# Kernel tuning notes

Measured on AMD Instinct MI355X. Metric: run time of the kernel, lower is better.

## Reference

```python
import jax, jax.numpy as jnp
import numpy as np
import math

N_NODES = 100000
N_EDGES = 3200000
IN_DIM = 256
HID_DIM = 256
OUT_DIM = 64
K1 = 2
P_DECAY = 1.0


def setup_inputs() -> dict:
    key = jax.random.key(0)
    k1, k2, k3, k4, k5, k6, k7 = jax.random.split(key, 7)
    x = jax.random.normal(k1, (N_NODES, IN_DIM), dtype=jnp.float32)
    edge_src = jax.random.randint(k2, (N_EDGES,), 0, N_NODES, dtype=jnp.int32)
    edge_dst = jax.random.randint(k3, (N_EDGES,), 0, N_NODES, dtype=jnp.int32)
    # Linear params (fc of conv1 and conv2), torch default init scale
    s1 = 1.0 / math.sqrt(IN_DIM)
    s2 = 1.0 / math.sqrt(HID_DIM)
    W1 = jax.random.uniform(k4, (IN_DIM, HID_DIM), jnp.float32, -s1, s1)
    b1 = jax.random.uniform(k5, (HID_DIM,), jnp.float32, -s1, s1)
    W2 = jax.random.uniform(k6, (HID_DIM, OUT_DIM), jnp.float32, -s2, s2)
    b2 = jax.random.uniform(k7, (OUT_DIM,), jnp.float32, -s2, s2)
    return {"x": x, "edge_src": edge_src, "edge_dst": edge_dst,
            "W1": W1, "b1": b1, "W2": W2, "b2": b2}


def _kprop_aggregate(x, src, dst, K, p, add_self_loops):
    """gcn_norm + K-hop propagation with exp(-p) decay per extra hop."""
    n = x.shape[0]
    if add_self_loops:
        loop = jnp.arange(n, dtype=src.dtype)
        src = jnp.concatenate([src, loop])
        dst = jnp.concatenate([dst, loop])
    # symmetric gcn normalization: w_ij = d_i^-1/2 * d_j^-1/2
    deg = jax.ops.segment_sum(jnp.ones_like(dst, dtype=x.dtype), dst, num_segments=n)
    dinv = jnp.where(deg > 0, jax.lax.rsqrt(jnp.maximum(deg, 1e-12)), 0.0)
    w = dinv[dst] * dinv[src]  # [E]
    coeff = 1.0
    for _ in range(K):
        msg = w[:, None] * x[src]                      # gather + scale  [E, D]
        x = jax.ops.segment_sum(msg, dst, num_segments=n) * coeff  # scatter-add [N, D]
        coeff = coeff * math.exp(-p)
    return x


def reference(x, edge_src, edge_dst, W1, b1, W2, b2):
    src = edge_src.astype(jnp.int32)
    dst = edge_dst.astype(jnp.int32)
    # conv1: KProp(K=2, gcn) -> no self loops in gcn_norm (add_self_loops = K==1)
    h = _kprop_aggregate(x, src, dst, K=K1, p=P_DECAY, add_self_loops=False)
    h = h @ W1 + b1
    h = jax.nn.selu(h)
    # dropout p=0.0 (eval-equivalent): identity
    # conv2: KProp(K=1, gcn) -> self loops added in gcn_norm
    h = _kprop_aggregate(h, src, dst, K=1, p=P_DECAY, add_self_loops=True)
    h = h @ W2 + b2
    return jax.nn.log_softmax(h, axis=1)
```

## Files before the change

kernel.cpp:

```cpp
#include <hip/hip_runtime.h>
#include <math.h>

static constexpr int IN_DIM_C  = 256;
static constexpr int HID_DIM_C = 256;
static constexpr int OUT_DIM_C = 64;
static constexpr float EXP_NEG1   = 0.36787944117144233f;
static constexpr float SELU_ALPHA = 1.6732632423543772f;
static constexpr float SELU_SCALE = 1.0507009873554805f;

static constexpr int NBLK  = 256;
static constexpr int NBUCK = 256;
static constexpr int BSH   = 9;
static constexpr int BMASK = (1 << BSH) - 1;

typedef __attribute__((ext_vector_type(4))) float f32x4;
typedef __attribute__((ext_vector_type(8))) short bf16x8;

__device__ __forceinline__ unsigned short bf1(float f) {
    unsigned int u = __float_as_uint(f);
    u = u + 0x7FFFu + ((u >> 16) & 1u);
    return (unsigned short)(u >> 16);
}
__device__ __forceinline__ unsigned int bfpack2(float lo, float hi) {
    return (unsigned int)bf1(lo) | ((unsigned int)bf1(hi) << 16);
}
__device__ __forceinline__ float fb(unsigned short h) {
    return __uint_as_float(((unsigned int)h) << 16);
}

__global__ __launch_bounds__(256) void k_hist(const int* __restrict__ dst,
                                              int* __restrict__ counts, int E) {
    __shared__ int hist[NBUCK];
    int tid = threadIdx.x, blk = blockIdx.x;
    hist[tid] = 0;
    __syncthreads();
    int ch = (E + NBLK - 1) / NBLK;
    int beg = blk * ch, end = min(beg + ch, E);
    for (int i = beg + tid; i < end; i += 256)
        atomicAdd(&hist[dst[i] >> BSH], 1);
    __syncthreads();
    counts[tid * NBLK + blk] = hist[tid];
}

__global__ void k_scan1(const int* __restrict__ in, int* __restrict__ out,
                        int* __restrict__ part, int n) {
    __shared__ int sm[256];
    int tid = threadIdx.x, idx = blockIdx.x * 256 + tid;
    int v = (idx < n) ? in[idx] : 0;
    sm[tid] = v; __syncthreads();
    #pragma unroll
    for (int o = 1; o < 256; o <<= 1) {
        int t = (tid >= o) ? sm[tid - o] : 0;
        __syncthreads();
        sm[tid] += t;
        __syncthreads();
    }
    if (idx < n) out[idx] = sm[tid] - v;
    if (tid == 255) part[blockIdx.x] = sm[255];
}

__global__ void k_scan2(int* __restrict__ part, int NB) {
    __shared__ int sm[512];
    int tid = threadIdx.x;
    int v = (tid < NB) ? part[tid] : 0;
    sm[tid] = v; __syncthreads();
    for (int o = 1; o < 512; o <<= 1) {
        int t = (tid >= o) ? sm[tid - o] : 0;
        __syncthreads();
        sm[tid] += t;
        __syncthreads();
    }
    if (tid < NB) part[tid] = sm[tid] - v;
}

__global__ void k_scan3b(int* __restrict__ v, const int* __restrict__ part, int n) {
    int idx = blockIdx.x * 256 + threadIdx.x;
    if (idx < n) v[idx] += part[idx >> 8];
}

__global__ __launch_bounds__(256) void k_scat(const int* __restrict__ src,
                                              const int* __restrict__ dst,
                                              const int* __restrict__ sc,
                                              unsigned int* __restrict__ spk, int E) {
    __shared__ int cur[NBUCK];
    int tid = threadIdx.x, blk = blockIdx.x;
    cur[tid] = sc[tid * NBLK + blk];
    __syncthreads();
    int ch = (E + NBLK - 1) / NBLK;
    int beg = blk * ch, end = min(beg + ch, E);
    for (int i = beg + tid; i < end; i += 256) {
        int d = dst[i];
        int b = d >> BSH;
        int slot = atomicAdd(&cur[b], 1);
        spk[slot] = ((unsigned int)src[i] << BSH) | (unsigned int)(d & BMASK);
    }
}

__global__ __launch_bounds__(256) void k_csr(const unsigned int* __restrict__ spk,
                                             const int* __restrict__ sc,
                                             int* __restrict__ csr,
                                             int* __restrict__ offsG,
                                             int* __restrict__ degG, int N, int E) {
    __shared__ int ldeg[512], loffs[512], sm[256];
    int tid = threadIdx.x, b = blockIdx.x;
    int start = sc[b * NBLK];
    int end   = (b == NBUCK - 1) ? E : sc[(b + 1) * NBLK];
    ldeg[tid] = 0; ldeg[tid + 256] = 0;
    __syncthreads();
    for (int i = start + tid; i < end; i += 256)
        atomicAdd(&ldeg[spk[i] & BMASK], 1);
    __syncthreads();
    int d0 = ldeg[2 * tid], d1 = ldeg[2 * tid + 1];
    int s = d0 + d1;
    sm[tid] = s; __syncthreads();
    #pragma unroll
    for (int o = 1; o < 256; o <<= 1) {
        int t = (tid >= o) ? sm[tid - o] : 0;
        __syncthreads();
        sm[tid] += t;
        __syncthreads();
    }
    int excl = sm[tid] - s;
    loffs[2 * tid] = excl;
    loffs[2 * tid + 1] = excl + d0;
    int node0 = b << BSH;
    int n0 = node0 + 2 * tid, n1 = n0 + 1;
    if (n0 < N) { offsG[n0] = start + excl;      degG[n0] = d0; }
    if (n1 < N) { offsG[n1] = start + excl + d0; degG[n1] = d1; }
    if (b == NBUCK - 1 && tid == 0) offsG[N] = E;
    __syncthreads();
    ldeg[tid] = 0; ldeg[tid + 256] = 0;
    __syncthreads();
    for (int i = start + tid; i < end; i += 256) {
        unsigned int pk = spk[i];
        int n = pk & BMASK;
        int k = atomicAdd(&ldeg[n], 1);
        csr[start + loffs[n] + k] = (int)(pk >> BSH);
    }
}

__global__ void k_dinv(const int* __restrict__ deg, float* __restrict__ dinv,
                       float* __restrict__ dinv2, int N) {
    int i = blockIdx.x * 256 + threadIdx.x;
    if (i < N) {
        int d = deg[i];
        dinv[i]  = (d > 0) ? rsqrtf((float)d) : 0.f;
        dinv2[i] = rsqrtf((float)(d + 1));
    }
}

__global__ void k_cvt(const float4* __restrict__ in, uint2* __restrict__ out, int n4) {
    int i = blockIdx.x * 256 + threadIdx.x;
    if (i < n4) {
        float4 v = in[i];
        uint2 o;
        o.x = bfpack2(v.x, v.y);
        o.y = bfpack2(v.z, v.w);
        out[i] = o;
    }
}

__global__ void k_packB(const float* __restrict__ W, unsigned short* __restrict__ Bp,
                        int K, int N) {
    int idx = blockIdx.x * 256 + threadIdx.x;
    if (idx >= K * N) return;
    int j = idx & 7;
    int l = (idx >> 3) & 63;
    int rest = idx >> 9;
    int KC = K >> 5;
    int c = rest % KC, t = rest / KC;
    int k = c * 32 + ((l >> 4) << 3) + j;
    int n = t * 16 + (l & 15);
    Bp[idx] = bf1(W[(size_t)k * N + n]);
}

__global__ void k_aggbf(const uint2* __restrict__ xin, uint2* __restrict__ yout,
                        const int* __restrict__ offs, const int* __restrict__ csr,
                        const float* __restrict__ dinv, float scl, int N) {
    int gw   = (blockIdx.x * blockDim.x + threadIdx.x) >> 6;
    int lane = threadIdx.x & 63;
    if (gw >= N) return;
    int beg = offs[gw], end = offs[gw + 1];
    float a0 = 0.f, a1 = 0.f, a2 = 0.f, a3 = 0.f;
    int e = beg;
    for (; e + 8 <= end; e += 8) {
        int s[8];
        #pragma unroll
        for (int j = 0; j < 8; ++j) s[j] = csr[e + j];
        float w[8];
        #pragma unroll
        for (int j = 0; j < 8; ++j) w[j] = dinv[s[j]];
        uint2 v[8];
        #pragma unroll
        for (int j = 0; j < 8; ++j) v[j] = xin[(size_t)s[j] * 64 + lane];
        #pragma unroll
        for (int j = 0; j < 8; ++j) {
            a0 = fmaf(w[j], __uint_as_float(v[j].x << 16), a0);
            a1 = fmaf(w[j], __uint_as_float(v[j].x & 0xFFFF0000u), a1);
            a2 = fmaf(w[j], __uint_as_float(v[j].y << 16), a2);
            a3 = fmaf(w[j], __uint_as_float(v[j].y & 0xFFFF0000u), a3);
        }
    }
    for (; e < end; ++e) {
        int s = csr[e];
        float w = dinv[s];
        uint2 v = xin[(size_t)s * 64 + lane];
        a0 = fmaf(w, __uint_as_float(v.x << 16), a0);
        a1 = fmaf(w, __uint_as_float(v.x & 0xFFFF0000u), a1);
        a2 = fmaf(w, __uint_as_float(v.y << 16), a2);
        a3 = fmaf(w, __uint_as_float(v.y & 0xFFFF0000u), a3);
    }
    float c = scl * dinv[gw];
    uint2 r;
    r.x = bfpack2(a0 * c, a1 * c);
    r.y = bfpack2(a2 * c, a3 * c);
    yout[(size_t)gw * 64 + lane] = r;
}

__device__ __forceinline__ float selu_f(float v) {
    return v > 0.f ? SELU_SCALE * v : SELU_SCALE * SELU_ALPHA * expm1f(v);
}

template <int K>
__global__ __launch_bounds__(256) void k_mgemm(
        const unsigned short* __restrict__ A,
        const unsigned short* __restrict__ Bp,
        const float* __restrict__ bias,
        unsigned short* __restrict__ Cb,
        int M, int Ncols, int act) {
    constexpr int KC = K >> 5;
    int wid  = threadIdx.x >> 6;
    int lane = threadIdx.x & 63;
    int m0   = blockIdx.x * 64 + wid * 16;
    int arow = m0 + (lane & 15);
    int kg   = lane >> 4;
    bf16x8 af[KC];
    bf16x8 zf = {0, 0, 0, 0, 0, 0, 0, 0};
    bool valid = arow < M;
    #pragma unroll
    for (int c = 0; c < KC; ++c) {
        if (valid) af[c] = *(const bf16x8*)&A[(size_t)arow * K + c * 32 + kg * 8];
        else       af[c] = zf;
    }
    int NT = Ncols >> 4;
    for (int t = 0; t < NT; ++t) {
        f32x4 acc = {0.f, 0.f, 0.f, 0.f};
        #pragma unroll
        for (int c = 0; c < KC; ++c) {
            bf16x8 bfv = *(const bf16x8*)&Bp[(((size_t)t * KC + c) * 64 + lane) * 8];
            acc = __builtin_amdgcn_mfma_f32_16x16x32_bf16(af[c], bfv, acc, 0, 0, 0);
        }
        int n = t * 16 + (lane & 15);
        float bv = bias ? bias[n] : 0.f;
        #pragma unroll
        for (int r = 0; r < 4; ++r) {
            int m = m0 + (lane >> 4) * 4 + r;
            if (m < M) {
                float v = acc[r] + bv;
                if (act) v = selu_f(v);
                Cb[(size_t)m * Ncols + n] = bf1(v);
            }
        }
    }
}

__global__ void k_agg64(const unsigned short* __restrict__ hw, float* __restrict__ out,
                        const int* __restrict__ offs, const int* __restrict__ csr,
                        const float* __restrict__ dinv2, const float* __restrict__ b2, int N) {
    int gw   = (blockIdx.x * blockDim.x + threadIdx.x) >> 6;
    int lane = threadIdx.x & 63;
    if (gw >= N) return;
    int beg = offs[gw], end = offs[gw + 1];
    float di = dinv2[gw];
    float acc = di * fb(hw[(size_t)gw * 64 + lane]);
    int e = beg;
    for (; e + 8 <= end; e += 8) {
        int s[8];
        #pragma unroll
        for (int j = 0; j < 8; ++j) s[j] = csr[e + j];
        float w[8];
        #pragma unroll
        for (int j = 0; j < 8; ++j) w[j] = dinv2[s[j]];
        unsigned short v[8];
        #pragma unroll
        for (int j = 0; j < 8; ++j) v[j] = hw[(size_t)s[j] * 64 + lane];
        #pragma unroll
        for (int j = 0; j < 8; ++j) acc = fmaf(w[j], fb(v[j]), acc);
    }
    for (; e < end; ++e) {
        int s = csr[e];
        acc = fmaf(dinv2[s], fb(hw[(size_t)s * 64 + lane]), acc);
    }
    acc = di * acc + b2[lane];
    float m = acc;
    #pragma unroll
    for (int o = 32; o > 0; o >>= 1) m = fmaxf(m, __shfl_xor(m, o));
    float ex = expf(acc - m);
    float s = ex;
    #pragma unroll
    for (int o = 32; o > 0; o >>= 1) s += __shfl_xor(s, o);
    out[(size_t)gw * 64 + lane] = acc - m - logf(s);
}

extern "C" void kernel_launch(void* const* d_in, const int* in_sizes, int n_in,
                              void* d_out, int out_size, void* d_ws, size_t ws_size,
                              hipStream_t stream) {
    const float* x    = (const float*)d_in[0];
    const int*   esrc = (const int*)d_in[1];
    const int*   edst = (const int*)d_in[2];
    const float* W1   = (const float*)d_in[3];
    const float* b1   = (const float*)d_in[4];
    const float* W2   = (const float*)d_in[5];
    const float* b2   = (const float*)d_in[6];

    const int N = in_sizes[0] / IN_DIM_C;
    const int E = in_sizes[1];

    char* p = (char*)d_ws;
    auto carve = [&](size_t bytes) -> char* {
        char* r = p; p += (bytes + 255) & ~(size_t)255; return r;
    };
    int*   deg    = (int*)carve((size_t)N * 4);
    int*   offs   = (int*)carve((size_t)(N + 1) * 4);
    float* dinv   = (float*)carve((size_t)N * 4);
    float* dinv2  = (float*)carve((size_t)N * 4);
    int*   counts = (int*)carve((size_t)NBUCK * NBLK * 4);
    int*   sc     = (int*)carve(((size_t)NBUCK * NBLK + 1) * 4);
    int*   part   = (int*)carve(512 * 4);
    unsigned int* spk = (unsigned int*)carve((size_t)E * 4);
    int*   csr    = (int*)carve((size_t)E * 4);
    unsigned short* buf0 = (unsigned short*)carve((size_t)N * 256 * 2);
    unsigned short* buf1 = (unsigned short*)carve((size_t)N * 256 * 2);
    unsigned short* buf2 = (unsigned short*)carve((size_t)N * 256 * 2);
    unsigned short* W1p  = (unsigned short*)carve((size_t)IN_DIM_C * HID_DIM_C * 2);
    unsigned short* W2p  = (unsigned short*)carve((size_t)HID_DIM_C * OUT_DIM_C * 2);

    const int NB = (N + 255) / 256;
    const int NC = NBUCK * NBLK;

    k_hist <<<NBLK, 256, 0, stream>>>(edst, counts, E);
    k_scan1<<<NC / 256, 256, 0, stream>>>(counts, sc, part, NC);
    k_scan2<<<1, 512, 0, stream>>>(part, NC / 256);
    k_scan3b<<<NC / 256, 256, 0, stream>>>(sc, part, NC);
    k_scat <<<NBLK, 256, 0, stream>>>(esrc, edst, sc, spk, E);
    k_csr  <<<NBUCK, 256, 0, stream>>>(spk, sc, csr, offs, deg, N, E);
    k_dinv <<<NB, 256, 0, stream>>>(deg, dinv, dinv2, N);

    int n4 = N * IN_DIM_C / 4;
    k_cvt<<<(n4 + 255) / 256, 256, 0, stream>>>((const float4*)x, (uint2*)buf0, n4);
    k_packB<<<(IN_DIM_C * HID_DIM_C + 255) / 256, 256, 0, stream>>>(W1, W1p, IN_DIM_C, HID_DIM_C);
    k_packB<<<(HID_DIM_C * OUT_DIM_C + 255) / 256, 256, 0, stream>>>(W2, W2p, HID_DIM_C, OUT_DIM_C);

    const int aggBlocks = (N + 3) / 4;
    k_aggbf<<<aggBlocks, 256, 0, stream>>>((const uint2*)buf0, (uint2*)buf1,
                                           offs, csr, dinv, 1.0f, N);
    k_aggbf<<<aggBlocks, 256, 0, stream>>>((const uint2*)buf1, (uint2*)buf2,
                                           offs, csr, dinv, EXP_NEG1, N);
    k_mgemm<256><<<(N + 63) / 64, 256, 0, stream>>>(buf2, W1p, b1, buf0, N, HID_DIM_C, 1);
    k_mgemm<256><<<(N + 63) / 64, 256, 0, stream>>>(buf0, W2p, nullptr, buf1, N, OUT_DIM_C, 0);
    k_agg64<<<aggBlocks, 256, 0, stream>>>(buf1, (float*)d_out, offs, csr, dinv2, b2, N);
}
```

Before: 910.8 us.

## Split bf16 aggregation into feature halves and fuse both GEMMs via LDS

Each 256-wide bf16 aggregation pass is now two launches, each gathering half of the feature columns (128 columns, one 32-bit word per lane). The goal is a smaller gathered working set that fits better in cache, at the cost of reading the CSR indices and degree weights twice. The two dense GEMMs are fused into one kernel: the SELU hidden tile stays in shared memory and feeds the second MFMA product directly. This avoids writing and re-reading the N×256 hidden activation through global memory. Each gather is now narrower (4 bytes per lane instead of 8), and the fused kernel uses about 33 KB of LDS per block, which may reduce occupancy.

After: 906.7 us. No clear change (-0.4%).

```diff
diff --git a/kernel.cpp b/kernel.cpp
--- a/kernel.cpp
+++ b/kernel.cpp
@@ -174,14 +174,16 @@
     Bp[idx] = bf1(W[(size_t)k * N + n]);
 }
 
-__global__ void k_aggbf(const uint2* __restrict__ xin, uint2* __restrict__ yout,
-                        const int* __restrict__ offs, const int* __restrict__ csr,
-                        const float* __restrict__ dinv, float scl, int N) {
+__global__ void k_agghalf(const unsigned int* __restrict__ xin,
+                          unsigned int* __restrict__ yout,
+                          const int* __restrict__ offs, const int* __restrict__ csr,
+                          const float* __restrict__ dinv, float scl, int N, int half) {
     int gw   = (blockIdx.x * blockDim.x + threadIdx.x) >> 6;
     int lane = threadIdx.x & 63;
     if (gw >= N) return;
     int beg = offs[gw], end = offs[gw + 1];
-    float a0 = 0.f, a1 = 0.f, a2 = 0.f, a3 = 0.f;
+    int off = half * 64 + lane;
+    float a0 = 0.f, a1 = 0.f;
     int e = beg;
     for (; e + 8 <= end; e += 8) {
         int s[8];
@@ -190,76 +192,85 @@
         float w[8];
         #pragma unroll
         for (int j = 0; j < 8; ++j) w[j] = dinv[s[j]];
-        uint2 v[8];
-        #pragma unroll
-        for (int j = 0; j < 8; ++j) v[j] = xin[(size_t)s[j] * 64 + lane];
+        unsigned int v[8];
+        #pragma unroll
+        for (int j = 0; j < 8; ++j) v[j] = xin[(size_t)s[j] * 128 + off];
         #pragma unroll
         for (int j = 0; j < 8; ++j) {
-            a0 = fmaf(w[j], __uint_as_float(v[j].x << 16), a0);
-            a1 = fmaf(w[j], __uint_as_float(v[j].x & 0xFFFF0000u), a1);
-            a2 = fmaf(w[j], __uint_as_float(v[j].y << 16), a2);
-            a3 = fmaf(w[j], __uint_as_float(v[j].y & 0xFFFF0000u), a3);
+            a0 = fmaf(w[j], __uint_as_float(v[j] << 16), a0);
+            a1 = fmaf(w[j], __uint_as_float(v[j] & 0xFFFF0000u), a1);
         }
     }
     for (; e < end; ++e) {
         int s = csr[e];
         float w = dinv[s];
-        uint2 v = xin[(size_t)s * 64 + lane];
-        a0 = fmaf(w, __uint_as_float(v.x << 16), a0);
-        a1 = fmaf(w, __uint_as_float(v.x & 0xFFFF0000u), a1);
-        a2 = fmaf(w, __uint_as_float(v.y << 16), a2);
-        a3 = fmaf(w, __uint_as_float(v.y & 0xFFFF0000u), a3);
+        unsigned int v = xin[(size_t)s * 128 + off];
+        a0 = fmaf(w, __uint_as_float(v << 16), a0);
+        a1 = fmaf(w, __uint_as_float(v & 0xFFFF0000u), a1);
     }
     float c = scl * dinv[gw];
-    uint2 r;
-    r.x = bfpack2(a0 * c, a1 * c);
-    r.y = bfpack2(a2 * c, a3 * c);
-    yout[(size_t)gw * 64 + lane] = r;
+    yout[(size_t)gw * 128 + off] = bfpack2(a0 * c, a1 * c);
 }
 
 __device__ __forceinline__ float selu_f(float v) {
     return v > 0.f ? SELU_SCALE * v : SELU_SCALE * SELU_ALPHA * expm1f(v);
 }
 
-template <int K>
-__global__ __launch_bounds__(256) void k_mgemm(
+__global__ __launch_bounds__(256) void k_fgemm(
         const unsigned short* __restrict__ A,
-        const unsigned short* __restrict__ Bp,
-        const float* __restrict__ bias,
+        const unsigned short* __restrict__ B1p,
+        const float* __restrict__ b1,
+        const unsigned short* __restrict__ B2p,
         unsigned short* __restrict__ Cb,
-        int M, int Ncols, int act) {
-    constexpr int KC = K >> 5;
+        int M) {
+    __shared__ unsigned short hs[64][264];
     int wid  = threadIdx.x >> 6;
     int lane = threadIdx.x & 63;
     int m0   = blockIdx.x * 64 + wid * 16;
     int arow = m0 + (lane & 15);
     int kg   = lane >> 4;
-    bf16x8 af[KC];
     bf16x8 zf = {0, 0, 0, 0, 0, 0, 0, 0};
+    bf16x8 af[8];
     bool valid = arow < M;
     #pragma unroll
-    for (int c = 0; c < KC; ++c) {
-        if (valid) af[c] = *(const bf16x8*)&A[(size_t)arow * K + c * 32 + kg * 8];
+    for (int c = 0; c < 8; ++c) {
+        if (valid) af[c] = *(const bf16x8*)&A[(size_t)arow * 256 + c * 32 + kg * 8];
         else       af[c] = zf;
     }
-    int NT = Ncols >> 4;
-    for (int t = 0; t < NT; ++t) {
+    #pragma unroll 4
+    for (int t = 0; t < 16; ++t) {
         f32x4 acc = {0.f, 0.f, 0.f, 0.f};
         #pragma unroll
-        for (int c = 0; c < KC; ++c) {
-            bf16x8 bfv = *(const bf16x8*)&Bp[(((size_t)t * KC + c) * 64 + lane) * 8];
+        for (int c = 0; c < 8; ++c) {
+            bf16x8 bfv = *(const bf16x8*)&B1p[(((size_t)t * 8 + c) * 64 + lane) * 8];
             acc = __builtin_amdgcn_mfma_f32_16x16x32_bf16(af[c], bfv, acc, 0, 0, 0);
         }
         int n = t * 16 + (lane & 15);
-        float bv = bias ? bias[n] : 0.f;
+        float bv = b1[n];
+        #pragma unroll
+        for (int r = 0; r < 4; ++r) {
+            int rl = wid * 16 + (lane >> 4) * 4 + r;
+            hs[rl][n] = bf1(selu_f(acc[r] + bv));
+        }
+    }
+    __syncthreads();
+    bf16x8 af2[8];
+    #pragma unroll
+    for (int c = 0; c < 8; ++c)
+        af2[c] = *(const bf16x8*)&hs[wid * 16 + (lane & 15)][c * 32 + kg * 8];
+    #pragma unroll
+    for (int t = 0; t < 4; ++t) {
+        f32x4 acc = {0.f, 0.f, 0.f, 0.f};
+        #pragma unroll
+        for (int c = 0; c < 8; ++c) {
+            bf16x8 bfv = *(const bf16x8*)&B2p[(((size_t)t * 8 + c) * 64 + lane) * 8];
+            acc = __builtin_amdgcn_mfma_f32_16x16x32_bf16(af2[c], bfv, acc, 0, 0, 0);
+        }
+        int n = t * 16 + (lane & 15);
         #pragma unroll
         for (int r = 0; r < 4; ++r) {
             int m = m0 + (lane >> 4) * 4 + r;
-            if (m < M) {
-                float v = acc[r] + bv;
-                if (act) v = selu_f(v);
-                Cb[(size_t)m * Ncols + n] = bf1(v);
-            }
+            if (m < M) Cb[(size_t)m * 64 + n] = bf1(acc[r]);
         }
     }
 }
@@ -352,11 +363,14 @@
     k_packB<<<(HID_DIM_C * OUT_DIM_C + 255) / 256, 256, 0, stream>>>(W2, W2p, HID_DIM_C, OUT_DIM_C);
 
     const int aggBlocks = (N + 3) / 4;
-    k_aggbf<<<aggBlocks, 256, 0, stream>>>((const uint2*)buf0, (uint2*)buf1,
-                                           offs, csr, dinv, 1.0f, N);
-    k_aggbf<<<aggBlocks, 256, 0, stream>>>((const uint2*)buf1, (uint2*)buf2,
-                                           offs, csr, dinv, EXP_NEG1, N);
-    k_mgemm<256><<<(N + 63) / 64, 256, 0, stream>>>(buf2, W1p, b1, buf0, N, HID_DIM_C, 1);
-    k_mgemm<256><<<(N + 63) / 64, 256, 0, stream>>>(buf0, W2p, nullptr, buf1, N, OUT_DIM_C, 0);
+    k_agghalf<<<aggBlocks, 256, 0, stream>>>((const unsigned int*)buf0, (unsigned int*)buf1,
+                                             offs, csr, dinv, 1.0f, N, 0);
+    k_agghalf<<<aggBlocks, 256, 0, stream>>>((const unsigned int*)buf0, (unsigned int*)buf1,
+                                             offs, csr, dinv, 1.0f, N, 1);
+    k_agghalf<<<aggBlocks, 256, 0, stream>>>((const unsigned int*)buf1, (unsigned int*)buf2,
+                                             offs, csr, dinv, EXP_NEG1, N, 0);
+    k_agghalf<<<aggBlocks, 256, 0, stream>>>((const unsigned int*)buf1, (unsigned int*)buf2,
+                                             offs, csr, dinv, EXP_NEG1, N, 1);
+    k_fgemm<<<(N + 63) / 64, 256, 0, stream>>>(buf2, W1p, b1, W2p, buf1, N);
     k_agg64<<<aggBlocks, 256, 0, stream>>>(buf1, (float*)d_out, offs, csr, dinv2, b2, N);
 }
```
